# Performance work log

Measured on AMD Instinct MI355X. Metric: run time of the kernel, lower is better.

The kernel has to match this reference:

```python
import jax, jax.numpy as jnp
import numpy as np

T, B, D, H = 2048, 2, 1024, 16
NH, DH = H // 2, D // H   # 8 heads per direction, d_head = 64
DFF = 4096


def layer_norm(x, g, b, eps=1e-5):
    mu = jnp.mean(x, axis=-1, keepdims=True)
    var = jnp.mean(jnp.square(x - mu), axis=-1, keepdims=True)
    return (x - mu) * jax.lax.rsqrt(var + eps) * g + b


def rel_shift(x):
    # x: [q, k, b, n] -> Transformer-XL relative shift
    q, k, b, n = x.shape
    x = jnp.concatenate([jnp.zeros((q, 1, b, n), x.dtype), x], axis=1)
    return x.reshape(k + 1, q, b, n)[1:].reshape(q, k, b, n)


def rel_attn(w, r, mask, qkv_w, r_w, r_w_bias, r_r_bias):
    # w: [T, B, D], r: [R, 1, D], mask: [T, T] bool (True = masked)
    t, b, _ = w.shape
    heads = jnp.einsum('tbd,ed->tbe', w, qkv_w)              # [T,B,3*NH*DH]
    q, k, v = jnp.split(heads, 3, axis=-1)
    q = q.reshape(t, b, NH, DH)
    k = k.reshape(t, b, NH, DH)
    v = v.reshape(t, b, NH, DH)
    rk = jnp.einsum('rd,ed->re', r[:, 0, :], r_w).reshape(-1, NH, DH)  # [R,NH,DH]
    AC = jnp.einsum('ibnd,jbnd->ijbn', q + r_w_bias, k)
    BD = rel_shift(jnp.einsum('ibnd,jnd->ijbn', q + r_r_bias, rk))
    score = (AC + BD) * (1.0 / np.sqrt(DH))
    score = jnp.where(mask[:, :, None, None], jnp.finfo(score.dtype).min, score)
    prob = jax.nn.softmax(score, axis=1)
    vec = jnp.einsum('ijbn,jbnd->ibnd', prob, v)
    return vec.reshape(t, b, NH * DH)


def setup_inputs() -> dict:
    key = jax.random.key(0)
    ks = jax.random.split(key, 24)
    s = 0.02
    causal = jnp.triu(jnp.ones((T, T), dtype=bool), k=1)
    return {
        'x': jax.random.normal(ks[0], (T, B, D), jnp.float32),
        'pos': jax.random.normal(ks[1], (T, 1, D), jnp.float32),
        'mask_fwd': causal,
        'mask_bwd': causal,
        'ln1_g': jnp.ones((D,), jnp.float32), 'ln1_b': jnp.zeros((D,), jnp.float32),
        'ln2_g': jnp.ones((D,), jnp.float32), 'ln2_b': jnp.zeros((D,), jnp.float32),
        'ln3_g': jnp.ones((D,), jnp.float32), 'ln3_b': jnp.zeros((D,), jnp.float32),
        'qkv_f': jax.random.normal(ks[2], (3 * NH * DH, D), jnp.float32) * s,
        'rnet_f': jax.random.normal(ks[3], (NH * DH, D), jnp.float32) * s,
        'rwb_f': jax.random.normal(ks[4], (NH, DH), jnp.float32) * s,
        'rrb_f': jax.random.normal(ks[5], (NH, DH), jnp.float32) * s,
        'qkv_b': jax.random.normal(ks[6], (3 * NH * DH, D), jnp.float32) * s,
        'rnet_b': jax.random.normal(ks[7], (NH * DH, D), jnp.float32) * s,
        'rwb_b': jax.random.normal(ks[8], (NH, DH), jnp.float32) * s,
        'rrb_b': jax.random.normal(ks[9], (NH, DH), jnp.float32) * s,
        'wo': jax.random.normal(ks[10], (D, D), jnp.float32) * s,
        'bo': jnp.zeros((D,), jnp.float32),
        'w1': jax.random.normal(ks[11], (DFF, D), jnp.float32) * s,
        'b1': jnp.zeros((DFF,), jnp.float32),
        'w2': jax.random.normal(ks[12], (D, DFF), jnp.float32) * s,
        'b2': jnp.zeros((D,), jnp.float32),
    }


def reference(x, pos, mask_fwd, mask_bwd,
              ln1_g, ln1_b, ln2_g, ln2_b, ln3_g, ln3_b,
              qkv_f, rnet_f, rwb_f, rrb_f,
              qkv_b, rnet_b, rwb_b, rrb_b,
              wo, bo, w1, b1, w2, b2):
    # --- bidirectional relative attention ---
    q_fwd = layer_norm(x, ln1_g, ln1_b)
    q_bwd = layer_norm(jnp.flip(x, axis=0), ln2_g, ln2_b)
    out_fwd = rel_attn(q_fwd, pos, mask_fwd, qkv_f, rnet_f, rwb_f, rrb_f)
    out_bwd = rel_attn(q_bwd, pos, mask_bwd, qkv_b, rnet_b, rwb_b, rrb_b)
    out = jnp.concatenate([out_fwd, jnp.flip(out_bwd, axis=0)], axis=-1)
    out = jnp.einsum('tbd,ed->tbe', out, wo) + bo
    h = x + out                     # postprocess_attn: dropout(id) + residual
    # --- feed forward: LN -> Linear -> ReLU -> Linear -> residual ---
    y = layer_norm(h, ln3_g, ln3_b)
    y = jax.nn.relu(jnp.einsum('tbd,fd->tbf', y, w1) + b1)
    y = jnp.einsum('tbf,df->tbd', y, w2) + b2
    return h + y
```

## Files before the change

kernel.cpp:

```cpp
#include <hip/hip_runtime.h>
#include <cstdint>
#include <cstddef>


typedef unsigned short ushort_t;
typedef __bf16 bf16x8 __attribute__((ext_vector_type(8)));
typedef float f32x4 __attribute__((ext_vector_type(4)));
typedef unsigned short us8 __attribute__((ext_vector_type(8)));
typedef unsigned short us4 __attribute__((ext_vector_type(4)));

#define DEV static __device__ __forceinline__

DEV ushort_t f2bf(float x) {
  union { float f; unsigned u; } v; v.f = x;
  unsigned r = (v.u + 0x7FFFu + ((v.u >> 16) & 1u)) >> 16;
  return (ushort_t)r;
}
DEV ushort_t f2bt(float x) {
  union { float f; unsigned u; } v; v.f = x;
  return (ushort_t)(v.u >> 16);
}
DEV float bf2f(ushort_t h) {
  union { unsigned u; float f; } v; v.u = ((unsigned)h) << 16;
  return v.f;
}
DEV float fexp2(float x) { float r; asm("v_exp_f32 %0, %1" : "=v"(r) : "v"(x)); return r; }
DEV f32x4 mfma16(bf16x8 a, bf16x8 b, f32x4 c) {
  return __builtin_amdgcn_mfma_f32_16x16x32_bf16(a, b, c, 0, 0, 0);
}
DEV void gld16(const void* g, void* l) {
  __builtin_amdgcn_global_load_lds((const __attribute__((address_space(1))) void*)g,
                                   (__attribute__((address_space(3))) void*)l,
                                   16, 0, 0);
}

constexpr float SCLQ = 0.125f * 1.44269504088896f;

constexpr size_t O_QKV_F  = 0;
constexpr size_t O_QKV_B  = 3145728;
constexpr size_t O_RNET_F = 6291456;
constexpr size_t O_RNET_B = 7340032;
constexpr size_t O_WO     = 8388608;
constexpr size_t O_W1     = 10485760;
constexpr size_t O_W2     = 18874368;
constexpr size_t O_RKREV_F= 27262976;
constexpr size_t O_RKREV_B= 29360128;
constexpr size_t O_QAC_F  = 31457280;
constexpr size_t O_QBD_F  = 35651584;
constexpr size_t O_KK_F   = 39845888;
constexpr size_t O_VT_F   = 44040192;
constexpr size_t O_QAC_B  = 48234496;
constexpr size_t O_QBD_B  = 52428800;
constexpr size_t O_KK_B   = 56623104;
constexpr size_t O_VT_B   = 60817408;
constexpr size_t O_H      = 65011712;
constexpr size_t O_LN3    = 81788928;
constexpr size_t ZONE     = 90177536;
constexpr size_t O_POS    = ZONE + 0;
constexpr size_t O_LN1    = ZONE + 4194304;
constexpr size_t O_LN2    = ZONE + 12582912;
constexpr size_t O_HEADS_F= ZONE + 20971520;
constexpr size_t O_HEADS_B= ZONE + 33554432;
constexpr size_t O_ACAT   = ZONE + 0;
constexpr size_t O_FFNM   = ZONE + 8388608;
constexpr size_t O_FPART  = O_QAC_F;

struct PrepArgs {
  const float* src[8];
  ushort_t* dst[8];
  int bstart[8];
  int cvt_blocks;
  const float* x;
  const float* g1; const float* b1;
  const float* g2; const float* b2;
  ushort_t* o1; ushort_t* o2;
};
__global__ __launch_bounds__(256)
void prep_k(PrepArgs a) {
  __shared__ float sbuf[8];
  const int bx = blockIdx.x;
  const int tid = threadIdx.x;
  if (bx < a.cvt_blocks) {
    int s = 0;
#pragma unroll
    for (int k = 1; k < 8; ++k) if (bx >= a.bstart[k]) s = k;
    int i = (bx - a.bstart[s]) * 256 + tid;
    float4 v = reinterpret_cast<const float4*>(a.src[s])[i];
    us4 o; o[0] = f2bf(v.x); o[1] = f2bf(v.y); o[2] = f2bf(v.z); o[3] = f2bf(v.w);
    reinterpret_cast<us4*>(a.dst[s])[i] = o;
    return;
  }
  const int row = bx - a.cvt_blocks;
  const float* xr = a.x + (size_t)row * 1024;
  float4 v = reinterpret_cast<const float4*>(xr)[tid];
  float s  = v.x + v.y + v.z + v.w;
  float s2 = v.x*v.x + v.y*v.y + v.z*v.z + v.w*v.w;
  for (int m = 32; m >= 1; m >>= 1) { s += __shfl_xor(s, m, 64); s2 += __shfl_xor(s2, m, 64); }
  int w = tid >> 6;
  if ((tid & 63) == 0) { sbuf[w] = s; sbuf[4 + w] = s2; }
  __syncthreads();
  float S  = sbuf[0] + sbuf[1] + sbuf[2] + sbuf[3];
  float S2 = sbuf[4] + sbuf[5] + sbuf[6] + sbuf[7];
  float mu  = S * (1.f / 1024.f);
  float var = S2 * (1.f / 1024.f) - mu * mu;
  float inv = rsqrtf(var + 1e-5f);
  int t = row >> 1, b = row & 1;
  size_t r2 = ((size_t)(2047 - t) * 2 + b) * 1024;
  float4 G1 = reinterpret_cast<const float4*>(a.g1)[tid];
  float4 B1 = reinterpret_cast<const float4*>(a.b1)[tid];
  float4 G2 = reinterpret_cast<const float4*>(a.g2)[tid];
  float4 B2 = reinterpret_cast<const float4*>(a.b2)[tid];
  float n0 = (v.x - mu) * inv, n1 = (v.y - mu) * inv, n2 = (v.z - mu) * inv, n3 = (v.w - mu) * inv;
  us4 aa, c;
  aa[0] = f2bf(n0 * G1.x + B1.x); aa[1] = f2bf(n1 * G1.y + B1.y);
  aa[2] = f2bf(n2 * G1.z + B1.z); aa[3] = f2bf(n3 * G1.w + B1.w);
  c[0] = f2bf(n0 * G2.x + B2.x); c[1] = f2bf(n1 * G2.y + B2.y);
  c[2] = f2bf(n2 * G2.z + B2.z); c[3] = f2bf(n3 * G2.w + B2.w);
  reinterpret_cast<us4*>(a.o1 + (size_t)row * 1024)[tid] = aa;
  reinterpret_cast<us4*>(a.o2 + r2)[tid] = c;
}

__global__ __launch_bounds__(256)
void ln_one_k(const float* __restrict__ x,
              const float* __restrict__ g1, const float* __restrict__ b1,
              ushort_t* __restrict__ o1) {
  __shared__ float sbuf[8];
  const int row = blockIdx.x;
  const int tid = threadIdx.x;
  const float* xr = x + (size_t)row * 1024;
  float4 v = reinterpret_cast<const float4*>(xr)[tid];
  float s  = v.x + v.y + v.z + v.w;
  float s2 = v.x*v.x + v.y*v.y + v.z*v.z + v.w*v.w;
  for (int m = 32; m >= 1; m >>= 1) { s += __shfl_xor(s, m, 64); s2 += __shfl_xor(s2, m, 64); }
  int w = tid >> 6;
  if ((tid & 63) == 0) { sbuf[w] = s; sbuf[4 + w] = s2; }
  __syncthreads();
  float S  = sbuf[0] + sbuf[1] + sbuf[2] + sbuf[3];
  float S2 = sbuf[4] + sbuf[5] + sbuf[6] + sbuf[7];
  float mu  = S * (1.f / 1024.f);
  float var = S2 * (1.f / 1024.f) - mu * mu;
  float inv = rsqrtf(var + 1e-5f);
  float4 G1 = reinterpret_cast<const float4*>(g1)[tid];
  float4 B1 = reinterpret_cast<const float4*>(b1)[tid];
  us4 a;
  a[0] = f2bf((v.x - mu) * inv * G1.x + B1.x);
  a[1] = f2bf((v.y - mu) * inv * G1.y + B1.y);
  a[2] = f2bf((v.z - mu) * inv * G1.z + B1.z);
  a[3] = f2bf((v.w - mu) * inv * G1.w + B1.w);
  reinterpret_cast<us4*>(o1 + (size_t)row * 1024)[tid] = a;
}

template <int EPI>
__global__ __launch_bounds__(256)
void gemm_bt(const ushort_t* __restrict__ A, const ushort_t* __restrict__ B,
             void* __restrict__ C, const float* __restrict__ bias,
             const float* __restrict__ resid, int M, int N, int K) {
  __shared__ ushort_t As[128 * 64];
  __shared__ ushort_t Bs[128 * 64];
  const int tid = threadIdx.x;
  const int lane = tid & 63;
  const int w = tid >> 6;
  const int wm = w >> 1, wn = w & 1;
  const int row0 = blockIdx.y * 128, col0 = blockIdx.x * 128;
  const int lr = lane & 15;
  const int lkb = (lane >> 4) * 8;
  const int rr = lane >> 3;
  const int scb = ((lane & 7) ^ rr) * 8;
  const f32x4 fz = {0.f, 0.f, 0.f, 0.f};
  f32x4 acc[4][4];
#pragma unroll
  for (int i = 0; i < 4; ++i)
#pragma unroll
    for (int j = 0; j < 4; ++j) acc[i][j] = fz;

  for (int k0 = 0; k0 < K; k0 += 64) {
    __syncthreads();
#pragma unroll
    for (int it = 0; it < 4; ++it) {
      int rbase = it * 32 + w * 8;
      gld16(A + (size_t)(row0 + rbase + rr) * K + k0 + scb, (char*)As + rbase * 128);
      gld16(B + (size_t)(col0 + rbase + rr) * K + k0 + scb, (char*)Bs + rbase * 128);
    }
    __syncthreads();
#pragma unroll
    for (int kk = 0; kk < 64; kk += 32) {
      bf16x8 af[4], bfr[4];
#pragma unroll
      for (int mi = 0; mi < 4; ++mi) {
        int r = wm * 64 + mi * 16 + lr;
        int off = (r * 128 + (kk + lkb) * 2) ^ ((r & 7) << 4);
        af[mi] = *reinterpret_cast<const bf16x8*>((char*)As + off);
      }
#pragma unroll
      for (int ni = 0; ni < 4; ++ni) {
        int r = wn * 64 + ni * 16 + lr;
        int off = (r * 128 + (kk + lkb) * 2) ^ ((r & 7) << 4);
        bfr[ni] = *reinterpret_cast<const bf16x8*>((char*)Bs + off);
      }
#pragma unroll
      for (int mi = 0; mi < 4; ++mi)
#pragma unroll
        for (int ni = 0; ni < 4; ++ni)
          acc[mi][ni] = mfma16(af[mi], bfr[ni], acc[mi][ni]);
    }
  }
#pragma unroll
  for (int mi = 0; mi < 4; ++mi)
#pragma unroll
    for (int ni = 0; ni < 4; ++ni)
#pragma unroll
      for (int r = 0; r < 4; ++r) {
        int row = row0 + wm * 64 + mi * 16 + (lane >> 4) * 4 + r;
        int col = col0 + wn * 64 + ni * 16 + lr;
        float v = acc[mi][ni][r];
        if (EPI == 0) {
          ((ushort_t*)C)[(size_t)row * N + col] = f2bf(v);
        } else if (EPI == 1) {
          v += bias[col]; v = v > 0.f ? v : 0.f;
          ((ushort_t*)C)[(size_t)row * N + col] = f2bf(v);
        } else {
          v += bias[col] + resid[(size_t)row * N + col];
          ((float*)C)[(size_t)row * N + col] = v;
        }
      }
}

__global__ __launch_bounds__(256)
void qkvrk_k(const ushort_t* __restrict__ A0, const ushort_t* __restrict__ A1,
             const ushort_t* __restrict__ A2,
             const ushort_t* __restrict__ B0, const ushort_t* __restrict__ B1,
             const ushort_t* __restrict__ B2, const ushort_t* __restrict__ B3,
             char* __restrict__ wsb,
             const float* __restrict__ rw0, const float* __restrict__ rr0,
             const float* __restrict__ rw1, const float* __restrict__ rr1) {
  const int id = (int)blockIdx.x;
  int z, bxx, byy;
  if (id < 768) {
    z = id / 384;
    int rem = id - z * 384;
    bxx = rem % 12;
    byy = rem / 12;
  } else {
    int id2 = id - 768;
    z = 2 + (id2 >> 6);
    int rem = id2 & 63;
    bxx = rem & 3;
    byy = rem >> 2;
  }
  const ushort_t* A = (z == 0) ? A0 : (z == 1) ? A1 : A2;
  const ushort_t* B = (z == 0) ? B0 : (z == 1) ? B1 : (z == 2) ? B2 : B3;

  __shared__ ushort_t As[128 * 64];
  __shared__ ushort_t Bs[128 * 64];
  const int tid = threadIdx.x;
  const int lane = tid & 63;
  const int w = tid >> 6;
  const int wm = w >> 1, wn = w & 1;
  const int row0 = byy * 128, col0 = bxx * 128;
  const int lr = lane & 15;
  const int lkb = (lane >> 4) * 8;
  const int rr = lane >> 3;
  const int scb = ((lane & 7) ^ rr) * 8;
  const f32x4 fz = {0.f, 0.f, 0.f, 0.f};
  f32x4 acc[4][4];
#pragma unroll
  for (int i = 0; i < 4; ++i)
#pragma unroll
    for (int j = 0; j < 4; ++j) acc[i][j] = fz;

  for (int k0 = 0; k0 < 1024; k0 += 64) {
    __syncthreads();
#pragma unroll
    for (int it = 0; it < 4; ++it) {
      int rbase = it * 32 + w * 8;
      gld16(A + (size_t)(row0 + rbase + rr) * 1024 + k0 + scb, (char*)As + rbase * 128);
      gld16(B + (size_t)(col0 + rbase + rr) * 1024 + k0 + scb, (char*)Bs + rbase * 128);
    }
    __syncthreads();
#pragma unroll
    for (int kk = 0; kk < 64; kk += 32) {
      bf16x8 af[4], bfr[4];
#pragma unroll
      for (int mi = 0; mi < 4; ++mi) {
        int r = wm * 64 + mi * 16 + lr;
        int off = (r * 128 + (kk + lkb) * 2) ^ ((r & 7) << 4);
        af[mi] = *reinterpret_cast<const bf16x8*>((char*)As + off);
      }
#pragma unroll
      for (int ni = 0; ni < 4; ++ni) {
        int r = wn * 64 + ni * 16 + lr;
        int off = (r * 128 + (kk + lkb) * 2) ^ ((r & 7) << 4);
        bfr[ni] = *reinterpret_cast<const bf16x8*>((char*)Bs + off);
      }
#pragma unroll
      for (int mi = 0; mi < 4; ++mi)
#pragma unroll
        for (int ni = 0; ni < 4; ++ni)
          acc[mi][ni] = mfma16(af[mi], bfr[ni], acc[mi][ni]);
    }
  }
  const int dirz = z & 1;
  const float* rwb = dirz ? rw1 : rw0;
  const float* rrb = dirz ? rr1 : rr0;
#pragma unroll
  for (int mi = 0; mi < 4; ++mi)
#pragma unroll
    for (int ni = 0; ni < 4; ++ni)
#pragma unroll
      for (int r = 0; r < 4; ++r) {
        int row = row0 + wm * 64 + mi * 16 + (lane >> 4) * 4 + r;
        int col = col0 + wn * 64 + ni * 16 + lr;
        float v = acc[mi][ni][r];
        if (z < 2) {
          int t = row >> 1, bb = row & 1;
          if (col < 512) {
            int nn = col >> 6, dh = col & 63;
            ushort_t* q_ac = (ushort_t*)(wsb + (dirz ? O_QAC_B : O_QAC_F));
            ushort_t* q_bd = (ushort_t*)(wsb + (dirz ? O_QBD_B : O_QBD_F));
            size_t o = ((size_t)(bb * 8 + nn) * 2048 + t) * 64 + dh;
            q_ac[o] = f2bf((v + rwb[col]) * SCLQ);
            q_bd[o] = f2bf((v + rrb[col]) * SCLQ);
          } else if (col < 1024) {
            int cc = col - 512;
            int nn = cc >> 6, dh = cc & 63;
            ushort_t* kout = (ushort_t*)(wsb + (dirz ? O_KK_B : O_KK_F));
            kout[((size_t)(bb * 8 + nn) * 2048 + t) * 64 + dh] = f2bf(v);
          } else {
            ushort_t* hv = (ushort_t*)(wsb + (dirz ? O_HEADS_B : O_HEADS_F));
            hv[(size_t)row * 1536 + col] = f2bf(v);
          }
        } else {
          ushort_t* rkrev = (ushort_t*)(wsb + (dirz ? O_RKREV_B : O_RKREV_F));
          int nn = col >> 6, dh = col & 63;
          rkrev[((size_t)nn * 2048 + (2047 - row)) * 64 + dh] = f2bf(v);
        }
      }
}

template <int EPI>
__global__ __launch_bounds__(256)
void gemm_bt2(const ushort_t* __restrict__ A0, const ushort_t* __restrict__ A1,
              const ushort_t* __restrict__ B0, const ushort_t* __restrict__ B1,
              void* __restrict__ C0, void* __restrict__ C1,
              int M, int N, int K, int lda, int ldb) {
  __shared__ ushort_t As[128 * 64];
  __shared__ ushort_t Bs[128 * 64];
  const ushort_t* A = blockIdx.z ? A1 : A0;
  const ushort_t* B = blockIdx.z ? B1 : B0;
  void* C = blockIdx.z ? (void*)C1 : (void*)C0;
  const int tid = threadIdx.x;
  const int lane = tid & 63;
  const int w = tid >> 6;
  const int wm = w >> 1, wn = w & 1;
  const int row0 = blockIdx.y * 128, col0 = blockIdx.x * 128;
  const int lr = lane & 15;
  const int lkb = (lane >> 4) * 8;
  const int rr = lane >> 3;
  const int scb = ((lane & 7) ^ rr) * 8;
  const f32x4 fz = {0.f, 0.f, 0.f, 0.f};
  f32x4 acc[4][4];
#pragma unroll
  for (int i = 0; i < 4; ++i)
#pragma unroll
    for (int j = 0; j < 4; ++j) acc[i][j] = fz;

  for (int k0 = 0; k0 < K; k0 += 64) {
    __syncthreads();
#pragma unroll
    for (int it = 0; it < 4; ++it) {
      int rbase = it * 32 + w * 8;
      gld16(A + (size_t)(row0 + rbase + rr) * lda + k0 + scb, (char*)As + rbase * 128);
      gld16(B + (size_t)(col0 + rbase + rr) * ldb + k0 + scb, (char*)Bs + rbase * 128);
    }
    __syncthreads();
#pragma unroll
    for (int kk = 0; kk < 64; kk += 32) {
      bf16x8 af[4], bfr[4];
#pragma unroll
      for (int mi = 0; mi < 4; ++mi) {
        int r = wm * 64 + mi * 16 + lr;
        int off = (r * 128 + (kk + lkb) * 2) ^ ((r & 7) << 4);
        af[mi] = *reinterpret_cast<const bf16x8*>((char*)As + off);
      }
#pragma unroll
      for (int ni = 0; ni < 4; ++ni) {
        int r = wn * 64 + ni * 16 + lr;
        int off = (r * 128 + (kk + lkb) * 2) ^ ((r & 7) << 4);
        bfr[ni] = *reinterpret_cast<const bf16x8*>((char*)Bs + off);
      }
#pragma unroll
      for (int mi = 0; mi < 4; ++mi)
#pragma unroll
        for (int ni = 0; ni < 4; ++ni)
          acc[mi][ni] = mfma16(af[mi], bfr[ni], acc[mi][ni]);
    }
  }
#pragma unroll
  for (int mi = 0; mi < 4; ++mi)
#pragma unroll
    for (int ni = 0; ni < 4; ++ni)
#pragma unroll
      for (int r = 0; r < 4; ++r) {
        int row = row0 + wm * 64 + mi * 16 + (lane >> 4) * 4 + r;
        int col = col0 + wn * 64 + ni * 16 + lr;
        float v = acc[mi][ni][r];
        if (EPI == 5) ((ushort_t*)C)[(size_t)row * N + col] = f2bf(v);
      }
}

template <int EPI>
__global__ __launch_bounds__(256)
void gemm64(const ushort_t* __restrict__ A0, const ushort_t* __restrict__ A1,
            const ushort_t* __restrict__ B0, const ushort_t* __restrict__ B1,
            void* __restrict__ C0, void* __restrict__ C1,
            const float* __restrict__ bias, const float* __restrict__ resid,
            int M, int N, int K) {
  __shared__ ushort_t As[64 * 64];
  __shared__ ushort_t Bs[128 * 64];
  const ushort_t* A = blockIdx.z ? A1 : A0;
  const ushort_t* B = blockIdx.z ? B1 : B0;
  void* C = blockIdx.z ? (void*)C1 : (void*)C0;
  const int tid = threadIdx.x;
  const int lane = tid & 63;
  const int w = tid >> 6;
  const int wm = w >> 1, wn = w & 1;
  const int row0 = blockIdx.y * 64, col0 = blockIdx.x * 128;
  const int lr = lane & 15;
  const int lkb = (lane >> 4) * 8;
  const int rr = lane >> 3;
  const int scb = ((lane & 7) ^ rr) * 8;
  const f32x4 fz = {0.f, 0.f, 0.f, 0.f};
  f32x4 acc[2][4];
#pragma unroll
  for (int i = 0; i < 2; ++i)
#pragma unroll
    for (int j = 0; j < 4; ++j) acc[i][j] = fz;

  for (int k0 = 0; k0 < K; k0 += 64) {
    __syncthreads();
#pragma unroll
    for (int it = 0; it < 2; ++it) {
      int rbase = it * 32 + w * 8;
      gld16(A + (size_t)(row0 + rbase + rr) * K + k0 + scb, (char*)As + rbase * 128);
    }
#pragma unroll
    for (int it = 0; it < 4; ++it) {
      int rbase = it * 32 + w * 8;
      gld16(B + (size_t)(col0 + rbase + rr) * K + k0 + scb, (char*)Bs + rbase * 128);
    }
    __syncthreads();
#pragma unroll
    for (int kk = 0; kk < 64; kk += 32) {
      bf16x8 af[2], bfr[4];
#pragma unroll
      for (int mi = 0; mi < 2; ++mi) {
        int r = wm * 32 + mi * 16 + lr;
        int off = (r * 128 + (kk + lkb) * 2) ^ ((r & 7) << 4);
        af[mi] = *reinterpret_cast<const bf16x8*>((char*)As + off);
      }
#pragma unroll
      for (int ni = 0; ni < 4; ++ni) {
        int r = wn * 64 + ni * 16 + lr;
        int off = (r * 128 + (kk + lkb) * 2) ^ ((r & 7) << 4);
        bfr[ni] = *reinterpret_cast<const bf16x8*>((char*)Bs + off);
      }
#pragma unroll
      for (int mi = 0; mi < 2; ++mi)
#pragma unroll
        for (int ni = 0; ni < 4; ++ni)
          acc[mi][ni] = mfma16(af[mi], bfr[ni], acc[mi][ni]);
    }
  }
#pragma unroll
  for (int mi = 0; mi < 2; ++mi)
#pragma unroll
    for (int ni = 0; ni < 4; ++ni)
#pragma unroll
      for (int r = 0; r < 4; ++r) {
        int row = row0 + wm * 32 + mi * 16 + (lane >> 4) * 4 + r;
        int col = col0 + wn * 64 + ni * 16 + lr;
        float v = acc[mi][ni][r];
        if (EPI == 2) {
          v += bias[col] + resid[(size_t)row * N + col];
          ((float*)C)[(size_t)row * N + col] = v;
        }
      }
}

__global__ __launch_bounds__(256)
void ffn2_red_k(const ushort_t* __restrict__ p0, const ushort_t* __restrict__ p1,
                const float* __restrict__ b2, const float* __restrict__ h,
                float* __restrict__ out) {
  const int row = blockIdx.x;
  const int tid = threadIdx.x;
  const size_t base = (size_t)row * 1024;
  us4 a = reinterpret_cast<const us4*>(p0 + base)[tid];
  us4 b = reinterpret_cast<const us4*>(p1 + base)[tid];
  float4 hv = reinterpret_cast<const float4*>(h + base)[tid];
  float4 bb = reinterpret_cast<const float4*>(b2)[tid];
  float4 o;
  o.x = bf2f(a[0]) + bf2f(b[0]) + hv.x + bb.x;
  o.y = bf2f(a[1]) + bf2f(b[1]) + hv.y + bb.y;
  o.z = bf2f(a[2]) + bf2f(b[2]) + hv.z + bb.z;
  o.w = bf2f(a[3]) + bf2f(b[3]) + hv.w + bb.w;
  reinterpret_cast<float4*>(out + base)[tid] = o;
}

__global__ __launch_bounds__(256)
void v_trans2_k(const ushort_t* __restrict__ hf, const ushort_t* __restrict__ hb2,
                char* __restrict__ wsb) {
  __shared__ float tile[64][65];
  const int dir = blockIdx.z;
  const ushort_t* heads = dir ? hb2 : hf;
  ushort_t* vt = (ushort_t*)(wsb + (dir ? O_VT_B : O_VT_F));
  int tt0 = blockIdx.x * 64;
  int bn = blockIdx.y;
  int b = bn >> 3, n = bn & 7;
  int tid = threadIdx.x;
#pragma unroll
  for (int i = 0; i < 16; ++i) {
    int rr = i * 4 + (tid >> 6);
    int cc = tid & 63;
    tile[rr][cc] = bf2f(heads[(size_t)((tt0 + rr) * 2 + b) * 1536 + 1024 + n * 64 + cc]);
  }
  __syncthreads();
#pragma unroll
  for (int i = 0; i < 16; ++i) {
    int dh = i * 4 + (tid >> 6);
    int tt = tid & 63;
    vt[((size_t)bn * 64 + dh) * 2048 + tt0 + tt] = f2bf(tile[tt][dh]);
  }
}

__global__ __launch_bounds__(256)
void attn_k(const char* __restrict__ wsb, ushort_t* __restrict__ outp) {
  __shared__ ushort_t Kbuf[2][64 * 64];
  __shared__ ushort_t Vbuf[2][64 * 64];
  __shared__ alignas(16) ushort_t Gs[4][16 * 84];
  __shared__ ushort_t Ps[4][1024];

  const int tid = threadIdx.x;
  const int lane = tid & 63;
  const int w = tid >> 6;
  const int il = lane & 15;
  const int g = lane >> 4;
  const int lkb = g * 8;
  const int rr = lane >> 3;
  const int scb = ((lane & 7) ^ rr) * 8;

  const int id = (int)(blockIdx.x + (blockIdx.y << 4) + (blockIdx.z << 8));
  const int xcd = id & 7;
  const int ord = id >> 3;
  const int pair = xcd * 4 + (ord & 3);
  const int bx = ord >> 2;
  const int bn = pair & 15;
  const int dir = pair >> 4;

  const ushort_t* qac  = (const ushort_t*)(wsb + (dir ? O_QAC_B : O_QAC_F));
  const ushort_t* qbd  = (const ushort_t*)(wsb + (dir ? O_QBD_B : O_QBD_F));
  const ushort_t* kkv  = (const ushort_t*)(wsb + (dir ? O_KK_B  : O_KK_F));
  const ushort_t* vtp  = (const ushort_t*)(wsb + (dir ? O_VT_B  : O_VT_F));
  const ushort_t* rkrev= (const ushort_t*)(wsb + (dir ? O_RKREV_B : O_RKREV_F));
  const int colbase = dir ? 512 : 0;

  const size_t hb = (size_t)bn * 2048;
  const size_t vbase = (size_t)bn * 64;
  const size_t nb = (size_t)(bn & 7) * 2048;
  const int b = bn >> 3;
  const int n = bn & 7;

  ushort_t* gw = Gs[w];
  char* pw = (char*)Ps[w];

  for (int half = 0; half < 2; ++half) {
    const int it = half ? bx : (31 - bx);
    const int i0 = it * 64;
    const int NT = it + 1;
    const int iw0 = i0 + w * 16;

    auto STAGE = [&](int bi, int j0) {
      ushort_t* kb = Kbuf[bi] + w * 512;
      ushort_t* vbp = Vbuf[bi] + w * 512;
      gld16(kkv + (hb + j0 + w * 8 + rr) * 64 + scb, kb);
      gld16(kkv + (hb + j0 + 32 + w * 8 + rr) * 64 + scb, kb + 2048);
      gld16(vtp + (vbase + w * 8 + rr) * 2048 + j0 + scb, vbp);
      gld16(vtp + (vbase + 32 + w * 8 + rr) * 2048 + j0 + scb, vbp + 2048);
    };

    bf16x8 qa[2], qb[2];
#pragma unroll
    for (int kf = 0; kf < 2; ++kf) {
      size_t off = (hb + iw0 + il) * 64 + kf * 32 + lkb;
      qa[kf] = *reinterpret_cast<const bf16x8*>(qac + off);
      qb[kf] = *reinterpret_cast<const bf16x8*>(qbd + off);
    }

    const f32x4 fz = {0.f, 0.f, 0.f, 0.f};
    f32x4 Oa[4];
#pragma unroll
    for (int nf = 0; nf < 4; ++nf) Oa[nf] = fz;
    float lsum = 0.f;

    STAGE(0, 0);
    __syncthreads();
    int cur = 0;
    for (int jt = 0; jt < NT; ++jt) {
      const int j0 = jt * 64;

      bf16x8 bd0[5], bd1[5];
      const int dbase = iw0 - j0 - 63;
#pragma unroll
      for (int ng = 0; ng < 5; ++ng) {
        int d = dbase + ng * 16 + il;
        d = d < 0 ? 0 : (d > 2047 ? 2047 : d);
        const ushort_t* bp = rkrev + (nb + d) * 64 + lkb;
        bd0[ng] = *reinterpret_cast<const bf16x8*>(bp);
        bd1[ng] = *reinterpret_cast<const bf16x8*>(bp + 32);
      }
      if (jt + 1 < NT) STAGE(cur ^ 1, j0 + 64);

      const ushort_t* Ks = Kbuf[cur];
      const ushort_t* Vs = Vbuf[cur];
      f32x4 S[4], G[5];
#pragma unroll
      for (int nf = 0; nf < 4; ++nf) S[nf] = fz;
#pragma unroll
      for (int ng = 0; ng < 5; ++ng) G[ng] = fz;
      __builtin_amdgcn_s_setprio(1);
#pragma unroll
      for (int kf = 0; kf < 2; ++kf)
#pragma unroll
        for (int nf = 0; nf < 4; ++nf) {
          int r = nf * 16 + il;
          int off = (r * 128 + (kf * 32 + lkb) * 2) ^ ((r & 7) << 4);
          S[nf] = mfma16(*reinterpret_cast<const bf16x8*>((char*)Ks + off), qa[kf], S[nf]);
        }
#pragma unroll
      for (int ng = 0; ng < 5; ++ng) {
        G[ng] = mfma16(bd0[ng], qb[0], G[ng]);
        G[ng] = mfma16(bd1[ng], qb[1], G[ng]);
      }
      __builtin_amdgcn_s_setprio(0);
#pragma unroll
      for (int ng = 0; ng < 5; ++ng) {
        us4 pk;
        pk[0] = f2bt(G[ng][0]); pk[1] = f2bt(G[ng][1]);
        pk[2] = f2bt(G[ng][2]); pk[3] = f2bt(G[ng][3]);
        *reinterpret_cast<us4*>(gw + il * 84 + ng * 16 + g * 4) = pk;
      }
      const bool full = (j0 + 63 <= iw0);
#pragma unroll
      for (int nf = 0; nf < 4; ++nf) {
        int c3 = il - (nf * 16 + g * 4 + 3) + 63;
        int base4 = c3 & ~3;
        int o = c3 & 3;
        const ushort_t* gp = gw + il * 84 + base4;
        uint64_t av = *reinterpret_cast<const uint64_t*>(gp);
        uint64_t bv2 = *reinterpret_cast<const uint64_t*>(gp + 4);
        uint64_t vv = o ? ((av >> (16 * o)) | (bv2 << (64 - 16 * o))) : av;
#pragma unroll
        for (int r = 0; r < 4; ++r) {
          int jl = nf * 16 + g * 4 + r;
          float sv = S[nf][r] + bf2f((ushort_t)(vv >> (16 * (3 - r))));
          if (!full) sv = (j0 + jl <= iw0 + il) ? sv : -1e30f;
          S[nf][r] = sv;
        }
      }
#pragma unroll
      for (int nf = 0; nf < 4; ++nf) {
        us4 pk;
#pragma unroll
        for (int r = 0; r < 4; ++r) {
          float p = fexp2(S[nf][r]);
          lsum += p;
          pk[r] = f2bt(p);
        }
        int off = (il * 128 + (nf * 16 + g * 4) * 2) ^ ((il & 7) << 4);
        *reinterpret_cast<us4*>(pw + off) = pk;
      }
      __builtin_amdgcn_s_setprio(1);
#pragma unroll
      for (int kf = 0; kf < 2; ++kf) {
        int poff = (il * 128 + (kf * 32 + lkb) * 2) ^ ((il & 7) << 4);
        bf16x8 pt = *reinterpret_cast<const bf16x8*>(pw + poff);
#pragma unroll
        for (int nf = 0; nf < 4; ++nf) {
          int r = nf * 16 + il;
          int voff = (r * 128 + (kf * 32 + lkb) * 2) ^ ((r & 7) << 4);
          Oa[nf] = mfma16(*reinterpret_cast<const bf16x8*>((char*)Vs + voff), pt, Oa[nf]);
        }
      }
      __builtin_amdgcn_s_setprio(0);
      __syncthreads();
      cur ^= 1;
    }
    lsum += __shfl_xor(lsum, 16, 64);
    lsum += __shfl_xor(lsum, 32, 64);
    float invl = 1.f / lsum;
    int ig = iw0 + il;
    int tout = dir ? (2047 - ig) : ig;
    size_t orow = ((size_t)tout * 2 + b) * 1024 + colbase + n * 64;
#pragma unroll
    for (int nf = 0; nf < 4; ++nf) {
      us4 pk;
#pragma unroll
      for (int r = 0; r < 4; ++r) pk[r] = f2bf(Oa[nf][r] * invl);
      *reinterpret_cast<us4*>(outp + orow + nf * 16 + g * 4) = pk;
    }
  }
}

extern "C" void kernel_launch(void* const* d_in, const int* in_sizes, int n_in,
                              void* d_out, int out_size, void* d_ws, size_t ws_size,
                              hipStream_t stream) {
  (void)in_sizes; (void)n_in; (void)out_size; (void)ws_size;
  const float* x    = (const float*)d_in[0];
  const float* pos  = (const float*)d_in[1];
  const float* ln1g = (const float*)d_in[4];
  const float* ln1b = (const float*)d_in[5];
  const float* ln2g = (const float*)d_in[6];
  const float* ln2b = (const float*)d_in[7];
  const float* ln3g = (const float*)d_in[8];
  const float* ln3b = (const float*)d_in[9];
  const float* qkvf = (const float*)d_in[10];
  const float* rnetf= (const float*)d_in[11];
  const float* rwbf = (const float*)d_in[12];
  const float* rrbf = (const float*)d_in[13];
  const float* qkvb = (const float*)d_in[14];
  const float* rnetb= (const float*)d_in[15];
  const float* rwbb = (const float*)d_in[16];
  const float* rrbb = (const float*)d_in[17];
  const float* wo   = (const float*)d_in[18];
  const float* bo   = (const float*)d_in[19];
  const float* w1   = (const float*)d_in[20];
  const float* b1   = (const float*)d_in[21];
  const float* w2   = (const float*)d_in[22];
  const float* b2   = (const float*)d_in[23];
  float* out = (float*)d_out;
  char* ws = (char*)d_ws;
  auto U = [&](size_t off) { return (ushort_t*)(ws + off); };

  PrepArgs pa;
  const float* srcs[8] = {qkvf, qkvb, rnetf, rnetb, wo, w1, w2, pos};
  size_t dsts[8] = {O_QKV_F, O_QKV_B, O_RNET_F, O_RNET_B, O_WO, O_W1, O_W2, O_POS};
  int bl[8] = {1536, 1536, 512, 512, 1024, 4096, 4096, 2048};
  int cum = 0;
  for (int s = 0; s < 8; ++s) {
    pa.src[s] = srcs[s];
    pa.dst[s] = U(dsts[s]);
    pa.bstart[s] = cum;
    cum += bl[s];
  }
  pa.cvt_blocks = cum;
  pa.x = x; pa.g1 = ln1g; pa.b1 = ln1b; pa.g2 = ln2g; pa.b2 = ln2b;
  pa.o1 = U(O_LN1); pa.o2 = U(O_LN2);
  prep_k<<<dim3(cum + 4096), dim3(256), 0, stream>>>(pa);

  qkvrk_k<<<dim3(896), dim3(256), 0, stream>>>(
      U(O_LN1), U(O_LN2), U(O_POS),
      U(O_QKV_F), U(O_QKV_B), U(O_RNET_F), U(O_RNET_B),
      ws, rwbf, rrbf, rwbb, rrbb);

  v_trans2_k<<<dim3(32, 16, 2), dim3(256), 0, stream>>>(U(O_HEADS_F), U(O_HEADS_B), ws);

  attn_k<<<dim3(16, 16, 2), dim3(256), 0, stream>>>(ws, U(O_ACAT));

  gemm64<2><<<dim3(8, 64, 1), dim3(256), 0, stream>>>(
      U(O_ACAT), U(O_ACAT), U(O_WO), U(O_WO), ws + O_H, ws + O_H,
      bo, x, 4096, 1024, 1024);

  ln_one_k<<<dim3(4096), dim3(256), 0, stream>>>((const float*)(ws + O_H), ln3g, ln3b, U(O_LN3));
  gemm_bt<1><<<dim3(32, 32), dim3(256), 0, stream>>>(U(O_LN3), U(O_W1), U(O_FFNM), b1, nullptr, 4096, 4096, 1024);

  ushort_t* part0 = U(O_FPART);
  ushort_t* part1 = U(O_FPART + 8388608);
  gemm_bt2<5><<<dim3(8, 32, 2), dim3(256), 0, stream>>>(
      U(O_FFNM), U(O_FFNM) + 2048, U(O_W2), U(O_W2) + 2048, part0, part1,
      4096, 1024, 2048, 4096, 4096);
  ffn2_red_k<<<dim3(4096), dim3(256), 0, stream>>>(
      part0, part1, b2, (const float*)(ws + O_H), out);
}
```

Before: 306.6 us.

## Write V transposed from QKV epilogue and use 128-row attention tiles

The QKV GEMM epilogue now writes V directly into the transposed per-head layout, which removes the separate v_trans2 kernel and its extra round trip through global memory. The attention kernel moves from 256-thread blocks that each handle two 64-row query tiles to 512-thread blocks (8 waves) that each handle one 128-row tile. K/V tiles staged in shared memory are shared by twice as many query rows, and waves whose rows sit above the causal diagonal skip the compute for a tile. The new V stores are strided by 2048 elements per element and so poorly coalesced. Grid balance also changes: 512 blocks with phase-ordered tile sizes replace the paired long/short tiles per block.

New measurement: 360.2 us. 1.17x slower.

```diff
diff --git a/kernel.cpp b/kernel.cpp
--- a/kernel.cpp
+++ b/kernel.cpp
@@ -326,8 +326,10 @@
             ushort_t* kout = (ushort_t*)(wsb + (dirz ? O_KK_B : O_KK_F));
             kout[((size_t)(bb * 8 + nn) * 2048 + t) * 64 + dh] = f2bf(v);
           } else {
-            ushort_t* hv = (ushort_t*)(wsb + (dirz ? O_HEADS_B : O_HEADS_F));
-            hv[(size_t)row * 1536 + col] = f2bf(v);
+            int cc = col - 1024;
+            int nn = cc >> 6, dh = cc & 63;
+            ushort_t* vt = (ushort_t*)(wsb + (dirz ? O_VT_B : O_VT_F));
+            vt[((size_t)(bb * 8 + nn) * 64 + dh) * 2048 + t] = f2bf(v);
           }
         } else {
           ushort_t* rkrev = (ushort_t*)(wsb + (dirz ? O_RKREV_B : O_RKREV_F));
@@ -506,38 +508,12 @@
   reinterpret_cast<float4*>(out + base)[tid] = o;
 }
 
-__global__ __launch_bounds__(256)
-void v_trans2_k(const ushort_t* __restrict__ hf, const ushort_t* __restrict__ hb2,
-                char* __restrict__ wsb) {
-  __shared__ float tile[64][65];
-  const int dir = blockIdx.z;
-  const ushort_t* heads = dir ? hb2 : hf;
-  ushort_t* vt = (ushort_t*)(wsb + (dir ? O_VT_B : O_VT_F));
-  int tt0 = blockIdx.x * 64;
-  int bn = blockIdx.y;
-  int b = bn >> 3, n = bn & 7;
-  int tid = threadIdx.x;
-#pragma unroll
-  for (int i = 0; i < 16; ++i) {
-    int rr = i * 4 + (tid >> 6);
-    int cc = tid & 63;
-    tile[rr][cc] = bf2f(heads[(size_t)((tt0 + rr) * 2 + b) * 1536 + 1024 + n * 64 + cc]);
-  }
-  __syncthreads();
-#pragma unroll
-  for (int i = 0; i < 16; ++i) {
-    int dh = i * 4 + (tid >> 6);
-    int tt = tid & 63;
-    vt[((size_t)bn * 64 + dh) * 2048 + tt0 + tt] = f2bf(tile[tt][dh]);
-  }
-}
-
-__global__ __launch_bounds__(256)
+__global__ __launch_bounds__(512)
 void attn_k(const char* __restrict__ wsb, ushort_t* __restrict__ outp) {
   __shared__ ushort_t Kbuf[2][64 * 64];
   __shared__ ushort_t Vbuf[2][64 * 64];
-  __shared__ alignas(16) ushort_t Gs[4][16 * 84];
-  __shared__ ushort_t Ps[4][1024];
+  __shared__ alignas(16) ushort_t Gs[8][16 * 84];
+  __shared__ ushort_t Ps[8][1024];
 
   const int tid = threadIdx.x;
   const int lane = tid & 63;
@@ -548,13 +524,16 @@
   const int rr = lane >> 3;
   const int scb = ((lane & 7) ^ rr) * 8;
 
-  const int id = (int)(blockIdx.x + (blockIdx.y << 4) + (blockIdx.z << 8));
-  const int xcd = id & 7;
-  const int ord = id >> 3;
-  const int pair = xcd * 4 + (ord & 3);
-  const int bx = ord >> 2;
-  const int bn = pair & 15;
-  const int dir = pair >> 4;
+  const int id = (int)blockIdx.x;
+  const int phase = id >> 8;
+  const int rem = id & 255;
+  const int xcd = rem & 7;
+  const int ord = rem >> 3;
+  const int combo = xcd * 4 + (ord & 3);
+  const int q = ord >> 2;
+  const int it = phase ? q : (15 - q);
+  const int bn = combo & 15;
+  const int dir = combo >> 4;
 
   const ushort_t* qac  = (const ushort_t*)(wsb + (dir ? O_QAC_B : O_QAC_F));
   const ushort_t* qbd  = (const ushort_t*)(wsb + (dir ? O_QBD_B : O_QBD_F));
@@ -572,41 +551,37 @@
   ushort_t* gw = Gs[w];
   char* pw = (char*)Ps[w];
 
-  for (int half = 0; half < 2; ++half) {
-    const int it = half ? bx : (31 - bx);
-    const int i0 = it * 64;
-    const int NT = it + 1;
-    const int iw0 = i0 + w * 16;
-
-    auto STAGE = [&](int bi, int j0) {
-      ushort_t* kb = Kbuf[bi] + w * 512;
-      ushort_t* vbp = Vbuf[bi] + w * 512;
-      gld16(kkv + (hb + j0 + w * 8 + rr) * 64 + scb, kb);
-      gld16(kkv + (hb + j0 + 32 + w * 8 + rr) * 64 + scb, kb + 2048);
-      gld16(vtp + (vbase + w * 8 + rr) * 2048 + j0 + scb, vbp);
-      gld16(vtp + (vbase + 32 + w * 8 + rr) * 2048 + j0 + scb, vbp + 2048);
-    };
-
-    bf16x8 qa[2], qb[2];
-#pragma unroll
-    for (int kf = 0; kf < 2; ++kf) {
-      size_t off = (hb + iw0 + il) * 64 + kf * 32 + lkb;
-      qa[kf] = *reinterpret_cast<const bf16x8*>(qac + off);
-      qb[kf] = *reinterpret_cast<const bf16x8*>(qbd + off);
-    }
-
-    const f32x4 fz = {0.f, 0.f, 0.f, 0.f};
-    f32x4 Oa[4];
-#pragma unroll
-    for (int nf = 0; nf < 4; ++nf) Oa[nf] = fz;
-    float lsum = 0.f;
-
-    STAGE(0, 0);
-    __syncthreads();
-    int cur = 0;
-    for (int jt = 0; jt < NT; ++jt) {
-      const int j0 = jt * 64;
-
+  const int i0 = it * 128;
+  const int NT = 2 * it + 2;
+  const int iw0 = i0 + w * 16;
+
+  auto STAGE = [&](int bi, int j0) {
+    gld16(kkv + (hb + j0 + w * 8 + rr) * 64 + scb, Kbuf[bi] + w * 512);
+    gld16(vtp + (vbase + w * 8 + rr) * 2048 + j0 + scb, Vbuf[bi] + w * 512);
+  };
+
+  bf16x8 qa[2], qb[2];
+#pragma unroll
+  for (int kf = 0; kf < 2; ++kf) {
+    size_t off = (hb + iw0 + il) * 64 + kf * 32 + lkb;
+    qa[kf] = *reinterpret_cast<const bf16x8*>(qac + off);
+    qb[kf] = *reinterpret_cast<const bf16x8*>(qbd + off);
+  }
+
+  const f32x4 fz = {0.f, 0.f, 0.f, 0.f};
+  f32x4 Oa[4];
+#pragma unroll
+  for (int nf = 0; nf < 4; ++nf) Oa[nf] = fz;
+  float lsum = 0.f;
+
+  STAGE(0, 0);
+  __syncthreads();
+  int cur = 0;
+  for (int jt = 0; jt < NT; ++jt) {
+    const int j0 = jt * 64;
+    if (jt + 1 < NT) STAGE(cur ^ 1, j0 + 64);
+
+    if (j0 <= iw0 + 15) {
       bf16x8 bd0[5], bd1[5];
       const int dbase = iw0 - j0 - 63;
 #pragma unroll
@@ -617,8 +592,6 @@
         bd0[ng] = *reinterpret_cast<const bf16x8*>(bp);
         bd1[ng] = *reinterpret_cast<const bf16x8*>(bp + 32);
       }
-      if (jt + 1 < NT) STAGE(cur ^ 1, j0 + 64);
-
       const ushort_t* Ks = Kbuf[cur];
       const ushort_t* Vs = Vbuf[cur];
       f32x4 S[4], G[5];
@@ -691,22 +664,22 @@
         }
       }
       __builtin_amdgcn_s_setprio(0);
-      __syncthreads();
-      cur ^= 1;
-    }
-    lsum += __shfl_xor(lsum, 16, 64);
-    lsum += __shfl_xor(lsum, 32, 64);
-    float invl = 1.f / lsum;
-    int ig = iw0 + il;
-    int tout = dir ? (2047 - ig) : ig;
-    size_t orow = ((size_t)tout * 2 + b) * 1024 + colbase + n * 64;
-#pragma unroll
-    for (int nf = 0; nf < 4; ++nf) {
-      us4 pk;
-#pragma unroll
-      for (int r = 0; r < 4; ++r) pk[r] = f2bf(Oa[nf][r] * invl);
-      *reinterpret_cast<us4*>(outp + orow + nf * 16 + g * 4) = pk;
-    }
+    }
+    __syncthreads();
+    cur ^= 1;
+  }
+  lsum += __shfl_xor(lsum, 16, 64);
+  lsum += __shfl_xor(lsum, 32, 64);
+  float invl = 1.f / lsum;
+  int ig = iw0 + il;
+  int tout = dir ? (2047 - ig) : ig;
+  size_t orow = ((size_t)tout * 2 + b) * 1024 + colbase + n * 64;
+#pragma unroll
+  for (int nf = 0; nf < 4; ++nf) {
+    us4 pk;
+#pragma unroll
+    for (int r = 0; r < 4; ++r) pk[r] = f2bf(Oa[nf][r] * invl);
+    *reinterpret_cast<us4*>(outp + orow + nf * 16 + g * 4) = pk;
   }
 }
 
@@ -761,9 +734,7 @@
       U(O_QKV_F), U(O_QKV_B), U(O_RNET_F), U(O_RNET_B),
       ws, rwbf, rrbf, rwbb, rrbb);
 
-  v_trans2_k<<<dim3(32, 16, 2), dim3(256), 0, stream>>>(U(O_HEADS_F), U(O_HEADS_B), ws);
-
-  attn_k<<<dim3(16, 16, 2), dim3(256), 0, stream>>>(ws, U(O_ACAT));
+  attn_k<<<dim3(512), dim3(512), 0, stream>>>(ws, U(O_ACAT));
 
   gemm64<2><<<dim3(8, 64, 1), dim3(256), 0, stream>>>(
       U(O_ACAT), U(O_ACAT), U(O_WO), U(O_WO), ws + O_H, ws + O_H,
```
